# Kernel tuning notes

Measured on AMD Instinct MI355X. Metric: run time of the kernel, lower is better.

The kernel has to match this reference:

```python
import jax, jax.numpy as jnp
import numpy as np

N, M, B, L, D = 100000, 256, 8, 128, 64
COORD_MAX = 1024


def setup_inputs() -> dict:
    key = jax.random.key(0)
    ks = jax.random.split(key, 9)
    # batch ids sorted so the original loop's centroid_offset == column index
    clu_b = jnp.sort(jax.random.randint(ks[0], (N, 1), 0, B))
    cen_b = jnp.sort(jax.random.randint(ks[1], (M, 1), 0, B))
    clu_xyz = jax.random.randint(ks[2], (N, 3), 0, COORD_MAX)
    cen_xyz = jax.random.randint(ks[3], (M, 3), 0, COORD_MAX)
    return {
        "cluster_coords": jnp.concatenate([clu_b, clu_xyz], axis=1).astype(jnp.int32),
        "centroid_coords": jnp.concatenate([cen_b, cen_xyz], axis=1).astype(jnp.int32),
        "cluster_feats": jax.random.normal(ks[4], (N, L), jnp.float32),
        "centroid_feats": jax.random.normal(ks[5], (M, L), jnp.float32),
        "centroid_conf": jax.random.uniform(ks[6], (M, 1), jnp.float32),
        "W": jax.random.normal(ks[7], (L, D), jnp.float32) * 0.05,
        "b": jax.random.normal(ks[8], (D,), jnp.float32) * 0.05,
    }


def reference(cluster_coords, centroid_coords, cluster_feats, centroid_feats,
              centroid_conf, W, b):
    # pointwise Conv3d(k=1) == linear on features
    clu = cluster_feats @ W + b                      # [N, D]
    nrm = jnp.maximum(jnp.linalg.norm(clu, axis=1, keepdims=True), 1e-12)
    clu = clu / nrm                                  # F.normalize(p=2, dim=1)
    cen = centroid_conf * (centroid_feats @ W + b)   # [M, D]

    # same-batch mask replaces the python loop + scatter
    valid = cluster_coords[:, 0][:, None] == centroid_coords[:, 0][None, :]  # [N, M]

    # pairwise L2 distance on spatial coords via squared expansion (exact for small ints)
    cc = cluster_coords[:, 1:].astype(jnp.float32)   # [N, 3]
    ec = centroid_coords[:, 1:].astype(jnp.float32)  # [M, 3]
    d2 = (jnp.sum(cc * cc, axis=1)[:, None]
          + jnp.sum(ec * ec, axis=1)[None, :]
          - 2.0 * cc @ ec.T)
    dist = jnp.maximum(jnp.sqrt(jnp.maximum(d2, 0.0)), 0.1)  # clamp(min=0.1)

    logits = jnp.where(valid, -dist, -jnp.inf)
    attn = jax.nn.softmax(logits, axis=-1)           # per-row over same-batch centroids
    attn = jnp.where(valid, attn, 0.0)               # rows w/ no centroids -> 0 (matches zeros init)

    out = (clu @ cen.T) * attn                       # [N, M]
    return out
```

## Files before the change

### kernel.cpp

```cpp
#include <hip/hip_runtime.h>
#include <stdint.h>


#define NN 100000
#define MM 256
#define LL 128
#define DD 64
#define NTILES (NN / 16)

typedef float f32x4 __attribute__((ext_vector_type(4)));
typedef __bf16 bf16x8 __attribute__((ext_vector_type(8)));
typedef __fp16 fp16x2 __attribute__((ext_vector_type(2)));

union U16x8 { uint4 u; bf16x8 v; unsigned short s[8]; };
union UH2 { unsigned int u; fp16x2 h; };

static __device__ __forceinline__ unsigned short f2bf(float f) {
  union { float f; unsigned int i; } t; t.f = f;
  unsigned int x = t.i;
  x += 0x7fffu + ((x >> 16) & 1u);
  return (unsigned short)(x >> 16);
}

__global__ __launch_bounds__(256) void prep_kernel(
    const int* __restrict__ cen_coords,
    const float* __restrict__ cen_feats,
    const float* __restrict__ conf,
    const float* __restrict__ W,
    const float* __restrict__ bvec,
    unsigned short* __restrict__ cen_ws,
    unsigned short* __restrict__ wt_ws,
    float4* __restrict__ cmeta_ws)
{
  int tid = threadIdx.x;
  if (blockIdx.x < 16) {
    int m = blockIdx.x * 16 + (tid >> 4);
    int c = tid & 15;
    float a0 = 0.f, a1 = 0.f, a2 = 0.f, a3 = 0.f;
    for (int l = 0; l < LL; l++) {
      float f = cen_feats[m * LL + l];
      const float* wr = W + l * DD + c;
      a0 += f * wr[0];  a1 += f * wr[16];
      a2 += f * wr[32]; a3 += f * wr[48];
    }
    float cf = conf[m];
    cen_ws[m * DD + c +  0] = f2bf(cf * (a0 + bvec[c +  0]));
    cen_ws[m * DD + c + 16] = f2bf(cf * (a1 + bvec[c + 16]));
    cen_ws[m * DD + c + 32] = f2bf(cf * (a2 + bvec[c + 32]));
    cen_ws[m * DD + c + 48] = f2bf(cf * (a3 + bvec[c + 48]));
  } else {
    for (int i = tid; i < LL * DD; i += 256) {
      int l = i >> 6, d = i & 63;
      wt_ws[d * LL + l] = f2bf(W[l * DD + d]);
    }
    {
      int4 cc = ((const int4*)cen_coords)[tid];
      float4 f;
      f.x = (float)cc.y + 4096.0f * (float)cc.x;
      f.y = (float)cc.z;
      f.z = (float)cc.w;
      f.w = 0.0f;
      cmeta_ws[tid] = f;
    }
  }
}

__global__ __launch_bounds__(256, 5) void main_kernel(
    const int4* __restrict__ clu_coords4,
    const float* __restrict__ feats,
    const float* __restrict__ bvec,
    const unsigned short* __restrict__ cen_ws,
    const unsigned short* __restrict__ wt_ws,
    const float4* __restrict__ cmeta,
    float* __restrict__ out)
{
  __shared__ __align__(16) unsigned short clu_s[4][16 * 72];
  __shared__ __align__(16) float4 cmeta_s[MM];

  int tid = threadIdx.x;
  cmeta_s[tid] = cmeta[tid];
  __syncthreads();

  int wave = tid >> 6, lane = tid & 63;
  int q = lane >> 4, c = lane & 15;
  int tile = blockIdx.x * 4 + wave;
  if (tile >= NTILES) return;

  const float4* fb = (const float4*)(feats + (size_t)(tile * 16 + c) * LL);
  float4 ff[8];
#pragma unroll
  for (int ks = 0; ks < 4; ks++) {
    ff[2 * ks]     = fb[ks * 8 + q * 2];
    ff[2 * ks + 1] = fb[ks * 8 + q * 2 + 1];
  }
  int4 rm = clu_coords4[tile * 16 + c];
  float rx = (float)rm.y + 4096.0f * (float)rm.x;
  float ry = (float)rm.z;
  float rz = (float)rm.w;

  f32x4 acc[4] = {{0,0,0,0},{0,0,0,0},{0,0,0,0},{0,0,0,0}};
  {
    const uint4* wb = (const uint4*)wt_ws;
#pragma unroll
    for (int ks = 0; ks < 4; ks++) {
      float4 f0 = ff[2 * ks], f1 = ff[2 * ks + 1];
      U16x8 a;
      a.v[0] = (__bf16)f0.x; a.v[1] = (__bf16)f0.y; a.v[2] = (__bf16)f0.z; a.v[3] = (__bf16)f0.w;
      a.v[4] = (__bf16)f1.x; a.v[5] = (__bf16)f1.y; a.v[6] = (__bf16)f1.z; a.v[7] = (__bf16)f1.w;
#pragma unroll
      for (int nt = 0; nt < 4; nt++) {
        U16x8 b; b.u = wb[(nt * 16 + c) * 16 + ks * 4 + q];
        acc[nt] = __builtin_amdgcn_mfma_f32_16x16x32_bf16(a.v, b.v, acc[nt], 0, 0, 0);
      }
    }
  }
#pragma unroll
  for (int nt = 0; nt < 4; nt++) {
    float bv = bvec[nt * 16 + c];
    acc[nt][0] += bv; acc[nt][1] += bv; acc[nt][2] += bv; acc[nt][3] += bv;
  }
  float inv_nrm[4];
#pragma unroll
  for (int r = 0; r < 4; r++) {
    float s = acc[0][r]*acc[0][r] + acc[1][r]*acc[1][r] + acc[2][r]*acc[2][r] + acc[3][r]*acc[3][r];
    s += __shfl_xor(s, 1); s += __shfl_xor(s, 2); s += __shfl_xor(s, 4); s += __shfl_xor(s, 8);
    inv_nrm[r] = 1.0f / fmaxf(sqrtf(s), 1e-12f);
  }
#pragma unroll
  for (int nt = 0; nt < 4; nt++)
#pragma unroll
    for (int r = 0; r < 4; r++) {
      union { __bf16 h; unsigned short s; } u;
      u.h = (__bf16)(acc[nt][r] * inv_nrm[r]);
      clu_s[wave][(q * 4 + r) * 72 + nt * 16 + c] = u.s;
    }

  __builtin_amdgcn_sched_barrier(0);

  const uint4* cb = (const uint4*)(clu_s[wave]);
  U16x8 a0, a1;
  a0.u = cb[c * 9 + q];
  a1.u = cb[c * 9 + 4 + q];

  float d2m = 1e30f;
#pragma unroll
  for (int mt = 0; mt < 16; mt++) {
#pragma unroll
    for (int r = 0; r < 4; r++) {
      float4 cm = cmeta_s[mt * 16 + q * 4 + r];
      float dx = rx - cm.x, dy = ry - cm.y, dz = rz - cm.z;
      d2m = fminf(d2m, dx * dx + dy * dy + dz * dz);
    }
  }
  d2m = fminf(d2m, __shfl_xor(d2m, 16));
  d2m = fminf(d2m, __shfl_xor(d2m, 32));
  float dmv = fmaxf(sqrtf(d2m), 0.1f);

  uint2 ep[16];
  float rsum = 0.f;
#pragma unroll
  for (int mt = 0; mt < 16; mt++) {
    float e[4];
#pragma unroll
    for (int r = 0; r < 4; r++) {
      float4 cm = cmeta_s[mt * 16 + q * 4 + r];
      float dx = rx - cm.x, dy = ry - cm.y, dz = rz - cm.z;
      float d = fmaxf(sqrtf(dx * dx + dy * dy + dz * dz), 0.1f);
      e[r] = __expf(dmv - d);
      rsum += e[r];
    }
    UH2 p0, p1;
    p0.h = __builtin_amdgcn_cvt_pkrtz(e[0], e[1]);
    p1.h = __builtin_amdgcn_cvt_pkrtz(e[2], e[3]);
    ep[mt].x = p0.u;
    ep[mt].y = p1.u;
  }
  rsum += __shfl_xor(rsum, 16);
  rsum += __shfl_xor(rsum, 32);
  float sc = (d2m < 4.0e6f) ? 1.0f / rsum : 0.f;

  const uint4* cenb = (const uint4*)cen_ws;
  float4* ob4 = (float4*)(out + (size_t)(tile * 16 + c) * MM) + q;
#pragma unroll
  for (int mt = 0; mt < 16; mt++) {
    U16x8 b0, b1;
    b0.u = cenb[(mt * 16 + c) * 8 + q];
    b1.u = cenb[(mt * 16 + c) * 8 + 4 + q];
    f32x4 dacc = {0, 0, 0, 0};
    dacc = __builtin_amdgcn_mfma_f32_16x16x32_bf16(b0.v, a0.v, dacc, 0, 0, 0);
    dacc = __builtin_amdgcn_mfma_f32_16x16x32_bf16(b1.v, a1.v, dacc, 0, 0, 0);
    UH2 p0, p1; p0.u = ep[mt].x; p1.u = ep[mt].y;
    float4 v;
    v.x = dacc[0] * ((float)p0.h[0] * sc);
    v.y = dacc[1] * ((float)p0.h[1] * sc);
    v.z = dacc[2] * ((float)p1.h[0] * sc);
    v.w = dacc[3] * ((float)p1.h[1] * sc);
    ob4[mt * 4] = v;
  }
}

extern "C" void kernel_launch(void* const* d_in, const int* in_sizes, int n_in,
                              void* d_out, int out_size, void* d_ws, size_t ws_size,
                              hipStream_t stream) {
  const int* clu_coords = (const int*)d_in[0];
  const int* cen_coords = (const int*)d_in[1];
  const float* clu_feats = (const float*)d_in[2];
  const float* cen_feats = (const float*)d_in[3];
  const float* conf      = (const float*)d_in[4];
  const float* W         = (const float*)d_in[5];
  const float* bvec      = (const float*)d_in[6];
  float* out = (float*)d_out;

  char* ws = (char*)d_ws;
  unsigned short* cen_ws = (unsigned short*)ws;
  unsigned short* wt_ws  = (unsigned short*)(ws + 32768);
  float4* cmeta_ws       = (float4*)(ws + 32768 + 16384);

  prep_kernel<<<17, 256, 0, stream>>>(cen_coords, cen_feats, conf, W, bvec,
                                      cen_ws, wt_ws, cmeta_ws);
  main_kernel<<<(NTILES + 3) / 4, 256, 0, stream>>>(
      (const int4*)clu_coords, clu_feats, bvec, cen_ws, wt_ws, cmeta_ws, out);
}
```

Before: 200.7 us.

## Stage centroid embeddings in swizzled LDS and restructure first GEMM epilogue

```diff
diff --git a/kernel.cpp b/kernel.cpp
--- a/kernel.cpp
+++ b/kernel.cpp
@@ -20,6 +20,12 @@
   unsigned int x = t.i;
   x += 0x7fffu + ((x >> 16) & 1u);
   return (unsigned short)(x >> 16);
+}
+
+static __device__ __forceinline__ unsigned int pk_bf16(float lo, float hi) {
+  unsigned int r;
+  asm("v_cvt_pk_bf16_f32 %0, %1, %2" : "=v"(r) : "v"(lo), "v"(hi));
+  return r;
 }
 
 __global__ __launch_bounds__(256) void prep_kernel(
@@ -65,7 +71,7 @@
   }
 }
 
-__global__ __launch_bounds__(256, 5) void main_kernel(
+__global__ __launch_bounds__(256, 3) void main_kernel(
     const int4* __restrict__ clu_coords4,
     const float* __restrict__ feats,
     const float* __restrict__ bvec,
@@ -74,66 +80,89 @@
     const float4* __restrict__ cmeta,
     float* __restrict__ out)
 {
+  __shared__ __align__(16) uint4 cen_s4[2048];
+  __shared__ __align__(16) float4 cmeta_s[MM];
   __shared__ __align__(16) unsigned short clu_s[4][16 * 72];
-  __shared__ __align__(16) float4 cmeta_s[MM];
 
   int tid = threadIdx.x;
-  cmeta_s[tid] = cmeta[tid];
-  __syncthreads();
-
   int wave = tid >> 6, lane = tid & 63;
-  int q = lane >> 4, c = lane & 15;
+  int q = lane >> 4, c = lane & 15, s = c & 7;
   int tile = blockIdx.x * 4 + wave;
-  if (tile >= NTILES) return;
-
-  const float4* fb = (const float4*)(feats + (size_t)(tile * 16 + c) * LL);
+  int tl = tile < NTILES ? tile : NTILES - 1;
+
+  const uint4* cg = (const uint4*)cen_ws;
+  uint4 st[8];
+#pragma unroll
+  for (int i = 0; i < 8; i++) {
+    int fl = tid + i * 256;
+    int g = (fl & ~7) | ((fl ^ (fl >> 3)) & 7);
+    st[i] = cg[g];
+  }
+
+  const float4* fb = (const float4*)(feats + (size_t)(tl * 16 + c) * LL);
   float4 ff[8];
 #pragma unroll
   for (int ks = 0; ks < 4; ks++) {
     ff[2 * ks]     = fb[ks * 8 + q * 2];
     ff[2 * ks + 1] = fb[ks * 8 + q * 2 + 1];
   }
+  const uint4* wb = (const uint4*)wt_ws;
+  uint4 wbv[16];
+#pragma unroll
+  for (int ks = 0; ks < 4; ks++)
+#pragma unroll
+    for (int nt = 0; nt < 4; nt++)
+      wbv[ks * 4 + nt] = wb[(nt * 16 + c) * 16 + ks * 4 + q];
+
+#pragma unroll
+  for (int i = 0; i < 8; i++) cen_s4[tid + i * 256] = st[i];
+  cmeta_s[tid] = cmeta[tid];
+  __syncthreads();
+  if (tile >= NTILES) return;
+
   int4 rm = clu_coords4[tile * 16 + c];
   float rx = (float)rm.y + 4096.0f * (float)rm.x;
   float ry = (float)rm.z;
   float rz = (float)rm.w;
+  const float4* bv4 = (const float4*)bvec;
+  float4 bb[4];
+#pragma unroll
+  for (int nt = 0; nt < 4; nt++) bb[nt] = bv4[nt * 4 + q];
 
   f32x4 acc[4] = {{0,0,0,0},{0,0,0,0},{0,0,0,0},{0,0,0,0}};
-  {
-    const uint4* wb = (const uint4*)wt_ws;
-#pragma unroll
-    for (int ks = 0; ks < 4; ks++) {
-      float4 f0 = ff[2 * ks], f1 = ff[2 * ks + 1];
-      U16x8 a;
-      a.v[0] = (__bf16)f0.x; a.v[1] = (__bf16)f0.y; a.v[2] = (__bf16)f0.z; a.v[3] = (__bf16)f0.w;
-      a.v[4] = (__bf16)f1.x; a.v[5] = (__bf16)f1.y; a.v[6] = (__bf16)f1.z; a.v[7] = (__bf16)f1.w;
-#pragma unroll
-      for (int nt = 0; nt < 4; nt++) {
-        U16x8 b; b.u = wb[(nt * 16 + c) * 16 + ks * 4 + q];
-        acc[nt] = __builtin_amdgcn_mfma_f32_16x16x32_bf16(a.v, b.v, acc[nt], 0, 0, 0);
-      }
+#pragma unroll
+  for (int ks = 0; ks < 4; ks++) {
+    float4 f0 = ff[2 * ks], f1 = ff[2 * ks + 1];
+    U16x8 a;
+    a.v[0] = (__bf16)f0.x; a.v[1] = (__bf16)f0.y; a.v[2] = (__bf16)f0.z; a.v[3] = (__bf16)f0.w;
+    a.v[4] = (__bf16)f1.x; a.v[5] = (__bf16)f1.y; a.v[6] = (__bf16)f1.z; a.v[7] = (__bf16)f1.w;
+#pragma unroll
+    for (int nt = 0; nt < 4; nt++) {
+      U16x8 b; b.u = wbv[ks * 4 + nt];
+      acc[nt] = __builtin_amdgcn_mfma_f32_16x16x32_bf16(b.v, a.v, acc[nt], 0, 0, 0);
     }
   }
 #pragma unroll
   for (int nt = 0; nt < 4; nt++) {
-    float bv = bvec[nt * 16 + c];
-    acc[nt][0] += bv; acc[nt][1] += bv; acc[nt][2] += bv; acc[nt][3] += bv;
-  }
-  float inv_nrm[4];
-#pragma unroll
-  for (int r = 0; r < 4; r++) {
-    float s = acc[0][r]*acc[0][r] + acc[1][r]*acc[1][r] + acc[2][r]*acc[2][r] + acc[3][r]*acc[3][r];
-    s += __shfl_xor(s, 1); s += __shfl_xor(s, 2); s += __shfl_xor(s, 4); s += __shfl_xor(s, 8);
-    inv_nrm[r] = 1.0f / fmaxf(sqrtf(s), 1e-12f);
-  }
+    acc[nt][0] += bb[nt][0]; acc[nt][1] += bb[nt][1];
+    acc[nt][2] += bb[nt][2]; acc[nt][3] += bb[nt][3];
+  }
+  float ns = 0.f;
 #pragma unroll
   for (int nt = 0; nt < 4; nt++)
 #pragma unroll
-    for (int r = 0; r < 4; r++) {
-      union { __bf16 h; unsigned short s; } u;
-      u.h = (__bf16)(acc[nt][r] * inv_nrm[r]);
-      clu_s[wave][(q * 4 + r) * 72 + nt * 16 + c] = u.s;
-    }
+    for (int r = 0; r < 4; r++) ns += acc[nt][r] * acc[nt][r];
+  ns += __shfl_xor(ns, 16);
+  ns += __shfl_xor(ns, 32);
+  float inv_nrm = 1.0f / fmaxf(sqrtf(ns), 1e-12f);
+
+#pragma unroll
+  for (int nt = 0; nt < 4; nt++) {
+    uint2 w;
+    w.x = pk_bf16(acc[nt][0] * inv_nrm, acc[nt][1] * inv_nrm);
+    w.y = pk_bf16(acc[nt][2] * inv_nrm, acc[nt][3] * inv_nrm);
+    *(uint2*)&clu_s[wave][c * 72 + nt * 16 + q * 4] = w;
+  }
 
   __builtin_amdgcn_sched_barrier(0);
 
@@ -179,13 +208,14 @@
   rsum += __shfl_xor(rsum, 32);
   float sc = (d2m < 4.0e6f) ? 1.0f / rsum : 0.f;
 
-  const uint4* cenb = (const uint4*)cen_ws;
   float4* ob4 = (float4*)(out + (size_t)(tile * 16 + c) * MM) + q;
+  int i0 = c * 8 + (q ^ s);
+  int i1 = c * 8 + ((q + 4) ^ s);
 #pragma unroll
   for (int mt = 0; mt < 16; mt++) {
     U16x8 b0, b1;
-    b0.u = cenb[(mt * 16 + c) * 8 + q];
-    b1.u = cenb[(mt * 16 + c) * 8 + 4 + q];
+    b0.u = cen_s4[mt * 128 + i0];
+    b1.u = cen_s4[mt * 128 + i1];
     f32x4 dacc = {0, 0, 0, 0};
     dacc = __builtin_amdgcn_mfma_f32_16x16x32_bf16(b0.v, a0.v, dacc, 0, 0, 0);
     dacc = __builtin_amdgcn_mfma_f32_16x16x32_bf16(b1.v, a1.v, dacc, 0, 0, 0);
```

After: 183.7 us. 8.5% less time.
